# Kernel optimization log

Measured on AMD Instinct MI355X. Metric: run time of the kernel, lower is better.

Reference implementation:

```python
import jax, jax.numpy as jnp
import numpy as np

N_NODES = 50000
N_EDGES = 800000
IN_DIM, HIDDEN, Z_DIM = 32, 64, 32


def gcn_conv(x, W, b, src, dst, n):
    """PyG-style GCNConv: h = D^{-1/2}(A+I)D^{-1/2} (x W) + b."""
    h = x @ W  # [N, out]
    loop = jnp.arange(n, dtype=src.dtype)
    s = jnp.concatenate([src, loop])  # add self-loops
    d = jnp.concatenate([dst, loop])
    deg = jax.ops.segment_sum(jnp.ones(s.shape, h.dtype), d, num_segments=n)
    dinv = jax.lax.rsqrt(jnp.maximum(deg, jnp.asarray(1.0, h.dtype)))
    norm = dinv[s] * dinv[d]                       # [E+N]
    msg = h[s] * norm[:, None]                     # gather + scale
    out = jax.ops.segment_sum(msg, d, num_segments=n)  # scatter-add
    return out + b


def setup_inputs() -> dict:
    key = jax.random.key(0)
    ks = jax.random.split(key, 8)
    sc = lambda fan_in: 1.0 / np.sqrt(fan_in)
    x = jax.random.normal(ks[0], (N_NODES, IN_DIM), jnp.float32)
    edge_index = jax.random.randint(ks[1], (2, N_EDGES), 0, N_NODES, jnp.int64)
    W1 = jax.random.normal(ks[2], (IN_DIM, HIDDEN), jnp.float32) * sc(IN_DIM)
    b1 = jnp.zeros((HIDDEN,), jnp.float32)
    W2 = jax.random.normal(ks[3], (HIDDEN, HIDDEN), jnp.float32) * sc(HIDDEN)
    b2 = jnp.zeros((HIDDEN,), jnp.float32)
    W_mu = jax.random.normal(ks[4], (HIDDEN, Z_DIM), jnp.float32) * sc(HIDDEN)
    b_mu = jnp.zeros((Z_DIM,), jnp.float32)
    W_lv = jax.random.normal(ks[5], (HIDDEN, Z_DIM), jnp.float32) * sc(HIDDEN)
    b_lv = jnp.zeros((Z_DIM,), jnp.float32)
    eps = jax.random.normal(ks[6], (N_NODES, Z_DIM), jnp.float32)
    return {"x": x, "edge_index": edge_index, "W1": W1, "b1": b1, "W2": W2,
            "b2": b2, "W_mu": W_mu, "b_mu": b_mu, "W_lv": W_lv, "b_lv": b_lv,
            "eps": eps}


def reference(x, edge_index, W1, b1, W2, b2, W_mu, b_mu, W_lv, b_lv, eps):
    src, dst = edge_index[0], edge_index[1]
    n = x.shape[0]
    h = jax.nn.relu(gcn_conv(x, W1, b1, src, dst, n))
    h = jax.nn.relu(gcn_conv(h, W2, b2, src, dst, n))
    # dropout p=0.0 -> identity
    mu = gcn_conv(h, W_mu, b_mu, src, dst, n)
    logvar = gcn_conv(h, W_lv, b_lv, src, dst, n)
    z = mu + jnp.exp(0.5 * logvar) * eps  # reparametrize
    return (z, mu, logvar)
```

## Files before the change

kernel.cpp:

```cpp
#include <hip/hip_runtime.h>
#include <math.h>

#define N_NODES 50000
#define N_EDGES 800000
#define IN_DIM 32
#define HIDDEN 64
#define Z_DIM 32
#define SCAN_B 256
#define NB_SCAN ((N_NODES + SCAN_B - 1) / SCAN_B)
#define N_XCD 8
#define NPX ((N_NODES + N_XCD - 1) / N_XCD)
#define SLICE 2048
#define N_SLICE ((N_EDGES + SLICE - 1) / SLICE)
#define SCAT_B (N_SLICE * N_XCD)
#define FB 1024
#define CPAD 16

__device__ __forceinline__ unsigned short f2bf(float f) {
    unsigned int u = __float_as_uint(f);
    u += 0x7fffu + ((u >> 16) & 1u);
    return (unsigned short)(u >> 16);
}

__device__ __forceinline__ int detect64(const int* raw) {
    int lane = threadIdx.x & 63;
    int odd = raw[2 * lane + 1];
    unsigned long long b = __ballot(odd != 0);
    return (b == 0ULL) ? 1 : 0;
}

__device__ __forceinline__ void fma8(float w, uint4 f, float acc[8]) {
    acc[0] = fmaf(w, __uint_as_float(f.x << 16),         acc[0]);
    acc[1] = fmaf(w, __uint_as_float(f.x & 0xffff0000u), acc[1]);
    acc[2] = fmaf(w, __uint_as_float(f.y << 16),         acc[2]);
    acc[3] = fmaf(w, __uint_as_float(f.y & 0xffff0000u), acc[3]);
    acc[4] = fmaf(w, __uint_as_float(f.z << 16),         acc[4]);
    acc[5] = fmaf(w, __uint_as_float(f.z & 0xffff0000u), acc[5]);
    acc[6] = fmaf(w, __uint_as_float(f.w << 16),         acc[6]);
    acc[7] = fmaf(w, __uint_as_float(f.w & 0xffff0000u), acc[7]);
}
__device__ __forceinline__ void mul8(float w, uint4 f, float acc[8]) {
    acc[0] = w * __uint_as_float(f.x << 16);
    acc[1] = w * __uint_as_float(f.x & 0xffff0000u);
    acc[2] = w * __uint_as_float(f.y << 16);
    acc[3] = w * __uint_as_float(f.y & 0xffff0000u);
    acc[4] = w * __uint_as_float(f.z << 16);
    acc[5] = w * __uint_as_float(f.z & 0xffff0000u);
    acc[6] = w * __uint_as_float(f.w << 16);
    acc[7] = w * __uint_as_float(f.w & 0xffff0000u);
}

__global__ void prep_a_kernel(const float* __restrict__ x, unsigned short* __restrict__ xb,
                              const void* __restrict__ raw, ushort2* __restrict__ ep0,
                              int* __restrict__ cnt) {
    int is64 = detect64((const int*)raw);
    int i = blockIdx.x * 256 + threadIdx.x;
    if (i < N_NODES * IN_DIM) xb[i] = f2bf(x[i]);
    if (i < N_NODES * CPAD) cnt[i] = 0;
    if (i < N_EDGES) {
        int s, d;
        if (is64) {
            s = (int)((const long long*)raw)[i];
            d = (int)((const long long*)raw)[N_EDGES + i];
        } else {
            s = ((const int*)raw)[i];
            d = ((const int*)raw)[N_EDGES + i];
        }
        ep0[i] = make_ushort2((unsigned short)s, (unsigned short)d);
    }
}

__global__ __launch_bounds__(256) void hist_kernel(const ushort2* __restrict__ ep0,
                                                   int* __restrict__ cnt,
                                                   unsigned short* __restrict__ rank) {
    int xcd = blockIdx.x % N_XCD;
    int sl  = blockIdx.x / N_XCD;
    int lo  = xcd * NPX, hi = lo + NPX;
    int base = sl * SLICE;
#pragma unroll
    for (int j = 0; j < SLICE / 256; j++) {
        int e = base + j * 256 + threadIdx.x;
        if (e < N_EDGES) {
            int d = ep0[e].y;
            if (d >= lo && d < hi)
                rank[e] = (unsigned short)atomicAdd(&cnt[(size_t)d * CPAD], 1);
        }
    }
}

__global__ void scan1_kernel(const int* __restrict__ cnt, int* __restrict__ pre,
                             int* __restrict__ bsum, float* __restrict__ dinv) {
    __shared__ int s[SCAN_B];
    int t = threadIdx.x;
    int g = blockIdx.x * SCAN_B + t;
    int v = (g < N_NODES) ? cnt[(size_t)g * CPAD] : 0;
    if (g < N_NODES) dinv[g] = rsqrtf((float)(v + 1));
    s[t] = v;
    __syncthreads();
    for (int o = 1; o < SCAN_B; o <<= 1) {
        int add = (t >= o) ? s[t - o] : 0;
        __syncthreads();
        s[t] += add;
        __syncthreads();
    }
    if (g < N_NODES) pre[g] = s[t] - v;
    if (t == SCAN_B - 1) bsum[blockIdx.x] = s[t];
}

#define BSUM_SCAN_PROLOGUE(bsum, sb, sx)                                    \
    {                                                                       \
        int t_ = threadIdx.x;                                               \
        int bv_ = (t_ < NB_SCAN) ? bsum[t_] : 0;                            \
        sb[t_] = bv_;                                                       \
        __syncthreads();                                                    \
        for (int o_ = 1; o_ < 256; o_ <<= 1) {                              \
            int a_ = (t_ >= o_) ? sb[t_ - o_] : 0;                          \
            __syncthreads();                                                \
            sb[t_] += a_;                                                   \
            __syncthreads();                                                \
        }                                                                   \
        sx[t_] = sb[t_] - bv_;                                              \
        __syncthreads();                                                    \
    }

__global__ __launch_bounds__(256) void scatter_kernel(
        const ushort2* __restrict__ ep0, const unsigned short* __restrict__ rank,
        const int* __restrict__ pre, const int* __restrict__ bsum,
        const float* __restrict__ dinv, int2* __restrict__ ep) {
    __shared__ int sb[256];
    __shared__ int sx[256];
    BSUM_SCAN_PROLOGUE(bsum, sb, sx)
    int base = blockIdx.x * SLICE;
#pragma unroll
    for (int j = 0; j < SLICE / 256; j++) {
        int e = base + j * 256 + threadIdx.x;
        if (e < N_EDGES) {
            ushort2 sd = ep0[e];
            int d = sd.y;
            int p = pre[d] + sx[d >> 8] + (int)rank[e];
            int s = sd.x;
            ep[p] = make_int2(s, __float_as_int(dinv[s]));
        }
    }
}

__device__ __forceinline__ void agg64(int e0, int e1, int2 pr,
                                      const int2* __restrict__ ep,
                                      const uint4* __restrict__ g4,
                                      int2* eb, int lane, int gsel, int c,
                                      float acc[8]) {
    for (int b0 = e0; b0 < e1; b0 += 64) {
        int cnt = e1 - b0; cnt = cnt > 64 ? 64 : cnt;
        eb[lane] = pr;
        for (int j = 0; j < cnt; j += 16) {
            int2 ew0 = eb[j + gsel];
            int2 ew1 = eb[j + 8 + gsel];
            uint4 f0 = g4[(size_t)ew0.x * 8 + c];
            uint4 f1 = g4[(size_t)ew1.x * 8 + c];
            fma8(__int_as_float(ew0.y), f0, acc);
            fma8(__int_as_float(ew1.y), f1, acc);
        }
        if (b0 + 64 < e1) {
            pr = make_int2(0, 0);
            int idx = b0 + 64 + lane;
            if (idx < e1) pr = ep[idx];
        }
    }
}

__device__ __forceinline__ void agg32(int e0, int e1, int2 pr,
                                      const int2* __restrict__ ep,
                                      const uint4* __restrict__ x4,
                                      int2* eb, int lane, int gsel, int c,
                                      float acc[8]) {
    for (int b0 = e0; b0 < e1; b0 += 64) {
        int cnt = e1 - b0; cnt = cnt > 64 ? 64 : cnt;
        eb[lane] = pr;
        for (int j = 0; j < cnt; j += 32) {
            int2 ew0 = eb[j + gsel];
            int2 ew1 = eb[j + 16 + gsel];
            uint4 f0 = x4[(size_t)ew0.x * 4 + c];
            uint4 f1 = x4[(size_t)ew1.x * 4 + c];
            fma8(__int_as_float(ew0.y), f0, acc);
            fma8(__int_as_float(ew1.y), f1, acc);
        }
        if (b0 + 64 < e1) {
            pr = make_int2(0, 0);
            int idx = b0 + 64 + lane;
            if (idx < e1) pr = ep[idx];
        }
    }
}

__global__ __launch_bounds__(256) void fused_layer32_kernel(
        const int* __restrict__ pre, const int* __restrict__ bsum,
        const int2* __restrict__ ep, const float* __restrict__ dinv,
        const unsigned short* __restrict__ xb,
        const float* __restrict__ W1, const float* __restrict__ b1,
        unsigned short* __restrict__ out) {
    __shared__ int sb[256];
    __shared__ int sx[256];
    __shared__ int2 ebuf[4][64];
    __shared__ float sq[4][32];
    BSUM_SCAN_PROLOGUE(bsum, sb, sx)
    int lane = threadIdx.x & 63;
    int wav  = threadIdx.x >> 6;
    int gsel = lane >> 2;
    int c    = lane & 3;
    const uint4* x4 = (const uint4*)xb;
    int2* eb = &ebuf[wav][0];
    float wcol[IN_DIM];
#pragma unroll
    for (int k = 0; k < IN_DIM; k++) wcol[k] = W1[k * 64 + lane];
    float bb = b1[lane];
    int wid = __builtin_amdgcn_readfirstlane((int)((blockIdx.x * blockDim.x + threadIdx.x) >> 6));
    int nw  = (gridDim.x * blockDim.x) >> 6;
    int v = wid;
    if (v >= N_NODES) return;
    int e0 = pre[v] + sx[v >> 8];
    int e1 = (v + 1 < N_NODES) ? pre[v + 1] + sx[(v + 1) >> 8] : N_EDGES;
    float dv = dinv[v];
    uint4 hv = x4[(size_t)v * 4 + c];
    int2 pr = make_int2(0, 0);
    if (lane < e1 - e0) pr = ep[e0 + lane];
    while (v < N_NODES) {
        int vn = v + nw;
        int e0n = 0, e1n = 0;
        float dvn = 0.0f;
        uint4 hvn = make_uint4(0, 0, 0, 0);
        int2 prn = make_int2(0, 0);
        if (vn < N_NODES) {
            e0n = pre[vn] + sx[vn >> 8];
            e1n = (vn + 1 < N_NODES) ? pre[vn + 1] + sx[(vn + 1) >> 8] : N_EDGES;
            dvn = dinv[vn];
            hvn = x4[(size_t)vn * 4 + c];
            if (lane < e1n - e0n) prn = ep[e0n + lane];
        }
        float sv = (gsel == 0) ? dv : 0.0f;
        float acc[8];
        mul8(sv, hv, acc);
        agg32(e0, e1, pr, ep, x4, eb, lane, gsel, c, acc);
#pragma unroll
        for (int i = 0; i < 8; i++) {
            acc[i] += __shfl_xor(acc[i], 4);
            acc[i] += __shfl_xor(acc[i], 8);
            acc[i] += __shfl_xor(acc[i], 16);
            acc[i] += __shfl_xor(acc[i], 32);
        }
        if (lane < 4) {
            float4* qd = (float4*)(&sq[wav][lane * 8]);
            qd[0] = make_float4(dv * acc[0], dv * acc[1], dv * acc[2], dv * acc[3]);
            qd[1] = make_float4(dv * acc[4], dv * acc[5], dv * acc[6], dv * acc[7]);
        }
        float o0 = bb, o1 = 0.0f, o2 = 0.0f, o3 = 0.0f;
        const float4* q4 = (const float4*)(&sq[wav][0]);
#pragma unroll
        for (int k = 0; k < IN_DIM / 4; k++) {
            float4 tq = q4[k];
            o0 = fmaf(tq.x, wcol[4 * k + 0], o0);
            o1 = fmaf(tq.y, wcol[4 * k + 1], o1);
            o2 = fmaf(tq.z, wcol[4 * k + 2], o2);
            o3 = fmaf(tq.w, wcol[4 * k + 3], o3);
        }
        float o = (o0 + o1) + (o2 + o3);
        out[(size_t)v * 64 + lane] = f2bf(fmaxf(o, 0.0f));
        v = vn; e0 = e0n; e1 = e1n; dv = dvn; hv = hvn; pr = prn;
    }
}

__global__ __launch_bounds__(256) void fused_layer64_kernel(
        const int* __restrict__ pre, const int* __restrict__ bsum,
        const int2* __restrict__ ep, const float* __restrict__ dinv,
        const unsigned short* __restrict__ g,
        const float* __restrict__ W, const float* __restrict__ bias,
        unsigned short* __restrict__ out) {
    __shared__ int sb[256];
    __shared__ int sx[256];
    __shared__ int2 ebuf[4][64];
    __shared__ float sq[4][64];
    BSUM_SCAN_PROLOGUE(bsum, sb, sx)
    int lane = threadIdx.x & 63;
    int wav  = threadIdx.x >> 6;
    int gsel = lane >> 3;
    int c    = lane & 7;
    const uint4* g4 = (const uint4*)g;
    int2* eb = &ebuf[wav][0];
    float wcol[HIDDEN];
#pragma unroll
    for (int k = 0; k < HIDDEN; k++) wcol[k] = W[k * 64 + lane];
    float bb = bias[lane];
    int wid = __builtin_amdgcn_readfirstlane((int)((blockIdx.x * blockDim.x + threadIdx.x) >> 6));
    int nw  = (gridDim.x * blockDim.x) >> 6;
    int v = wid;
    if (v >= N_NODES) return;
    int e0 = pre[v] + sx[v >> 8];
    int e1 = (v + 1 < N_NODES) ? pre[v + 1] + sx[(v + 1) >> 8] : N_EDGES;
    float dv = dinv[v];
    uint4 hv = g4[(size_t)v * 8 + c];
    int2 pr = make_int2(0, 0);
    if (lane < e1 - e0) pr = ep[e0 + lane];
    while (v < N_NODES) {
        int vn = v + nw;
        int e0n = 0, e1n = 0;
        float dvn = 0.0f;
        uint4 hvn = make_uint4(0, 0, 0, 0);
        int2 prn = make_int2(0, 0);
        if (vn < N_NODES) {
            e0n = pre[vn] + sx[vn >> 8];
            e1n = (vn + 1 < N_NODES) ? pre[vn + 1] + sx[(vn + 1) >> 8] : N_EDGES;
            dvn = dinv[vn];
            hvn = g4[(size_t)vn * 8 + c];
            if (lane < e1n - e0n) prn = ep[e0n + lane];
        }
        float sv = (gsel == 0) ? dv : 0.0f;
        float acc[8];
        mul8(sv, hv, acc);
        agg64(e0, e1, pr, ep, g4, eb, lane, gsel, c, acc);
#pragma unroll
        for (int i = 0; i < 8; i++) {
            acc[i] += __shfl_xor(acc[i], 8);
            acc[i] += __shfl_xor(acc[i], 16);
            acc[i] += __shfl_xor(acc[i], 32);
        }
        if (lane < 8) {
            float4* qd = (float4*)(&sq[wav][lane * 8]);
            qd[0] = make_float4(dv * acc[0], dv * acc[1], dv * acc[2], dv * acc[3]);
            qd[1] = make_float4(dv * acc[4], dv * acc[5], dv * acc[6], dv * acc[7]);
        }
        float o0 = bb, o1 = 0.0f, o2 = 0.0f, o3 = 0.0f;
        const float4* q4 = (const float4*)(&sq[wav][0]);
#pragma unroll
        for (int k = 0; k < HIDDEN / 4; k++) {
            float4 tq = q4[k];
            o0 = fmaf(tq.x, wcol[4 * k + 0], o0);
            o1 = fmaf(tq.y, wcol[4 * k + 1], o1);
            o2 = fmaf(tq.z, wcol[4 * k + 2], o2);
            o3 = fmaf(tq.w, wcol[4 * k + 3], o3);
        }
        float o = (o0 + o1) + (o2 + o3);
        out[(size_t)v * 64 + lane] = f2bf(fmaxf(o, 0.0f));
        v = vn; e0 = e0n; e1 = e1n; dv = dvn; hv = hvn; pr = prn;
    }
}

__global__ __launch_bounds__(256) void fused_head_kernel(
        const int* __restrict__ pre, const int* __restrict__ bsum,
        const int2* __restrict__ ep, const float* __restrict__ dinv,
        const unsigned short* __restrict__ g,
        const float* __restrict__ Wmu, const float* __restrict__ Wlv,
        const float* __restrict__ bmu, const float* __restrict__ blv,
        const float* __restrict__ eps, float* __restrict__ outz) {
    __shared__ int sb[256];
    __shared__ int sx[256];
    __shared__ int2 ebuf[4][64];
    __shared__ float sq[4][64];
    BSUM_SCAN_PROLOGUE(bsum, sb, sx)
    int lane = threadIdx.x & 63;
    int wav  = threadIdx.x >> 6;
    int gsel = lane >> 3;
    int c    = lane & 7;
    int f = lane & 31;
    bool hi = lane >= 32;
    const uint4* g4 = (const uint4*)g;
    int2* eb = &ebuf[wav][0];
    float wcol[HIDDEN];
#pragma unroll
    for (int k = 0; k < HIDDEN; k++)
        wcol[k] = hi ? Wlv[k * 32 + f] : Wmu[k * 32 + f];
    float bb = hi ? blv[f] : bmu[f];
    float* z  = outz;
    float* mu = outz + (size_t)N_NODES * Z_DIM;
    float* lv = outz + 2 * (size_t)N_NODES * Z_DIM;
    int wid = __builtin_amdgcn_readfirstlane((int)((blockIdx.x * blockDim.x + threadIdx.x) >> 6));
    int nw  = (gridDim.x * blockDim.x) >> 6;
    int v = wid;
    if (v >= N_NODES) return;
    int e0 = pre[v] + sx[v >> 8];
    int e1 = (v + 1 < N_NODES) ? pre[v + 1] + sx[(v + 1) >> 8] : N_EDGES;
    float dv = dinv[v];
    uint4 hv = g4[(size_t)v * 8 + c];
    int2 pr = make_int2(0, 0);
    if (lane < e1 - e0) pr = ep[e0 + lane];
    while (v < N_NODES) {
        int vn = v + nw;
        int e0n = 0, e1n = 0;
        float dvn = 0.0f;
        uint4 hvn = make_uint4(0, 0, 0, 0);
        int2 prn = make_int2(0, 0);
        if (vn < N_NODES) {
            e0n = pre[vn] + sx[vn >> 8];
            e1n = (vn + 1 < N_NODES) ? pre[vn + 1] + sx[(vn + 1) >> 8] : N_EDGES;
            dvn = dinv[vn];
            hvn = g4[(size_t)vn * 8 + c];
            if (lane < e1n - e0n) prn = ep[e0n + lane];
        }
        float sv = (gsel == 0) ? dv : 0.0f;
        float acc[8];
        mul8(sv, hv, acc);
        agg64(e0, e1, pr, ep, g4, eb, lane, gsel, c, acc);
#pragma unroll
        for (int i = 0; i < 8; i++) {
            acc[i] += __shfl_xor(acc[i], 8);
            acc[i] += __shfl_xor(acc[i], 16);
            acc[i] += __shfl_xor(acc[i], 32);
        }
        if (lane < 8) {
            float4* qd = (float4*)(&sq[wav][lane * 8]);
            qd[0] = make_float4(dv * acc[0], dv * acc[1], dv * acc[2], dv * acc[3]);
            qd[1] = make_float4(dv * acc[4], dv * acc[5], dv * acc[6], dv * acc[7]);
        }
        float m0 = bb, m1 = 0.0f, m2 = 0.0f, m3 = 0.0f;
        const float4* q4 = (const float4*)(&sq[wav][0]);
#pragma unroll
        for (int k = 0; k < HIDDEN / 4; k++) {
            float4 tq = q4[k];
            m0 = fmaf(tq.x, wcol[4 * k + 0], m0);
            m1 = fmaf(tq.y, wcol[4 * k + 1], m1);
            m2 = fmaf(tq.z, wcol[4 * k + 2], m2);
            m3 = fmaf(tq.w, wcol[4 * k + 3], m3);
        }
        float m = (m0 + m1) + (m2 + m3);
        float ev = eps[(size_t)v * Z_DIM + f];
        float t  = expf(0.5f * m) * ev;
        float tlo = __shfl(t, lane | 32);
        size_t o = (size_t)v * Z_DIM + f;
        if (!hi) { mu[o] = m; z[o] = m + tlo; }
        else     { lv[o] = m; }
        v = vn; e0 = e0n; e1 = e1n; dv = dvn; hv = hvn; pr = prn;
    }
}

extern "C" void kernel_launch(void* const* d_in, const int* in_sizes, int n_in,
                              void* d_out, int out_size, void* d_ws, size_t ws_size,
                              hipStream_t stream) {
    const float* x   = (const float*)d_in[0];
    const void*  ei  = d_in[1];
    const float* W1  = (const float*)d_in[2];
    const float* b1  = (const float*)d_in[3];
    const float* W2  = (const float*)d_in[4];
    const float* b2  = (const float*)d_in[5];
    const float* Wmu = (const float*)d_in[6];
    const float* bmu = (const float*)d_in[7];
    const float* Wlv = (const float*)d_in[8];
    const float* blv = (const float*)d_in[9];
    const float* eps = (const float*)d_in[10];
    float* out = (float*)d_out;
    (void)in_sizes; (void)n_in; (void)out_size; (void)ws_size;

    char* ws = (char*)d_ws;
    size_t off = 0;
    auto alloc = [&](size_t bytes) -> void* {
        void* p = ws + off;
        off += (bytes + 255) & ~(size_t)255;
        return p;
    };
    int2*           ep     = (int2*)alloc(sizeof(int2) * N_EDGES);
    ushort2*        ep0    = (ushort2*)alloc(sizeof(ushort2) * N_EDGES);
    unsigned short* rank   = (unsigned short*)alloc(sizeof(short) * N_EDGES);
    int*            pre    = (int*)alloc(sizeof(int) * (N_NODES + 1));
    int*            cnt    = (int*)alloc(sizeof(int) * (size_t)N_NODES * CPAD);
    float*          dinv   = (float*)alloc(sizeof(float) * N_NODES);
    int*            bsum   = (int*)alloc(sizeof(int) * 256);
    unsigned short* xb     = (unsigned short*)alloc(sizeof(short) * (size_t)N_NODES * IN_DIM);
    unsigned short* G      = (unsigned short*)alloc(sizeof(short) * (size_t)N_NODES * HIDDEN);
    unsigned short* H      = (unsigned short*)alloc(sizeof(short) * (size_t)N_NODES * HIDDEN);

    prep_a_kernel<<<(N_NODES * IN_DIM + 255) / 256, 256, 0, stream>>>(x, xb, ei, ep0, cnt);
    hist_kernel<<<SCAT_B, 256, 0, stream>>>(ep0, cnt, rank);
    scan1_kernel<<<NB_SCAN, SCAN_B, 0, stream>>>(cnt, pre, bsum, dinv);
    scatter_kernel<<<N_SLICE, 256, 0, stream>>>(ep0, rank, pre, bsum, dinv, ep);
    fused_layer32_kernel<<<FB, 256, 0, stream>>>(pre, bsum, ep, dinv, xb, W1, b1, H);
    fused_layer64_kernel<<<FB, 256, 0, stream>>>(pre, bsum, ep, dinv, H, W2, b2, G);
    fused_head_kernel<<<FB, 256, 0, stream>>>(pre, bsum, ep, dinv, G, Wmu, Wlv, bmu, blv, eps, out);
}
```

Measured before the change: 249.1 us.

## Map multiple nodes per wavefront and finalize row pointers in a separate scan kernel

Each layer kernel used to process one node per wavefront in a grid-stride loop, staging edges through LDS. Now a sub-group of lanes (4 or 8) handles one node, so each wave covers 8 or 16 nodes, with edge indices broadcast by shuffles. The dense transform is batched over those nodes with weights held in LDS instead of registers. A new scan23 kernel finalizes global row pointers once, so the per-block bsum prefix-scan prologue in every consumer kernel is removed. This targets low lane utilization on low-degree nodes and the repeated scans, at the cost of load imbalance from the per-wave max degree and one extra launch.

```diff
diff --git a/kernel.cpp b/kernel.cpp
--- a/kernel.cpp
+++ b/kernel.cpp
@@ -13,8 +13,14 @@
 #define SLICE 2048
 #define N_SLICE ((N_EDGES + SLICE - 1) / SLICE)
 #define SCAT_B (N_SLICE * N_XCD)
-#define FB 1024
 #define CPAD 16
+
+#define NPW64 8
+#define NPB64 (4 * NPW64)
+#define FB64 ((N_NODES + NPB64 - 1) / NPB64)
+#define NPW32 16
+#define NPB32 (4 * NPW32)
+#define FB32 ((N_NODES + NPB32 - 1) / NPB32)
 
 __device__ __forceinline__ unsigned short f2bf(float f) {
     unsigned int u = __float_as_uint(f);
@@ -88,7 +94,7 @@
     }
 }
 
-__global__ void scan1_kernel(const int* __restrict__ cnt, int* __restrict__ pre,
+__global__ void scan1_kernel(const int* __restrict__ cnt, int* __restrict__ rowptr,
                              int* __restrict__ bsum, float* __restrict__ dinv) {
     __shared__ int s[SCAN_B];
     int t = threadIdx.x;
@@ -103,330 +109,309 @@
         s[t] += add;
         __syncthreads();
     }
-    if (g < N_NODES) pre[g] = s[t] - v;
+    if (g < N_NODES) rowptr[g] = s[t] - v;
     if (t == SCAN_B - 1) bsum[blockIdx.x] = s[t];
 }
 
-#define BSUM_SCAN_PROLOGUE(bsum, sb, sx)                                    \
-    {                                                                       \
-        int t_ = threadIdx.x;                                               \
-        int bv_ = (t_ < NB_SCAN) ? bsum[t_] : 0;                            \
-        sb[t_] = bv_;                                                       \
-        __syncthreads();                                                    \
-        for (int o_ = 1; o_ < 256; o_ <<= 1) {                              \
-            int a_ = (t_ >= o_) ? sb[t_ - o_] : 0;                          \
-            __syncthreads();                                                \
-            sb[t_] += a_;                                                   \
-            __syncthreads();                                                \
-        }                                                                   \
-        sx[t_] = sb[t_] - bv_;                                              \
-        __syncthreads();                                                    \
-    }
+__global__ void scan23_kernel(int* __restrict__ rowptr, const int* __restrict__ bsum) {
+    __shared__ int s[256];
+    int t = threadIdx.x;
+    int v = (t < NB_SCAN) ? bsum[t] : 0;
+    s[t] = v;
+    __syncthreads();
+    for (int o = 1; o < 256; o <<= 1) {
+        int add = (t >= o) ? s[t - o] : 0;
+        __syncthreads();
+        s[t] += add;
+        __syncthreads();
+    }
+    int excl = s[blockIdx.x] - bsum[blockIdx.x];
+    int g = blockIdx.x * SCAN_B + t;
+    if (g < N_NODES) rowptr[g] += excl;
+    if (g == 0) rowptr[N_NODES] = N_EDGES;
+}
 
 __global__ __launch_bounds__(256) void scatter_kernel(
         const ushort2* __restrict__ ep0, const unsigned short* __restrict__ rank,
-        const int* __restrict__ pre, const int* __restrict__ bsum,
-        const float* __restrict__ dinv, int2* __restrict__ ep) {
-    __shared__ int sb[256];
-    __shared__ int sx[256];
-    BSUM_SCAN_PROLOGUE(bsum, sb, sx)
+        const int* __restrict__ rowptr, const float* __restrict__ dinv,
+        int2* __restrict__ ep) {
     int base = blockIdx.x * SLICE;
 #pragma unroll
     for (int j = 0; j < SLICE / 256; j++) {
         int e = base + j * 256 + threadIdx.x;
         if (e < N_EDGES) {
             ushort2 sd = ep0[e];
-            int d = sd.y;
-            int p = pre[d] + sx[d >> 8] + (int)rank[e];
+            int p = rowptr[sd.y] + (int)rank[e];
             int s = sd.x;
             ep[p] = make_int2(s, __float_as_int(dinv[s]));
         }
     }
 }
 
-__device__ __forceinline__ void agg64(int e0, int e1, int2 pr,
-                                      const int2* __restrict__ ep,
-                                      const uint4* __restrict__ g4,
-                                      int2* eb, int lane, int gsel, int c,
-                                      float acc[8]) {
-    for (int b0 = e0; b0 < e1; b0 += 64) {
-        int cnt = e1 - b0; cnt = cnt > 64 ? 64 : cnt;
-        eb[lane] = pr;
-        for (int j = 0; j < cnt; j += 16) {
-            int2 ew0 = eb[j + gsel];
-            int2 ew1 = eb[j + 8 + gsel];
-            uint4 f0 = g4[(size_t)ew0.x * 8 + c];
-            uint4 f1 = g4[(size_t)ew1.x * 8 + c];
-            fma8(__int_as_float(ew0.y), f0, acc);
-            fma8(__int_as_float(ew1.y), f1, acc);
-        }
-        if (b0 + 64 < e1) {
-            pr = make_int2(0, 0);
-            int idx = b0 + 64 + lane;
-            if (idx < e1) pr = ep[idx];
-        }
-    }
-}
-
-__device__ __forceinline__ void agg32(int e0, int e1, int2 pr,
-                                      const int2* __restrict__ ep,
-                                      const uint4* __restrict__ x4,
-                                      int2* eb, int lane, int gsel, int c,
-                                      float acc[8]) {
-    for (int b0 = e0; b0 < e1; b0 += 64) {
-        int cnt = e1 - b0; cnt = cnt > 64 ? 64 : cnt;
-        eb[lane] = pr;
-        for (int j = 0; j < cnt; j += 32) {
-            int2 ew0 = eb[j + gsel];
-            int2 ew1 = eb[j + 16 + gsel];
-            uint4 f0 = x4[(size_t)ew0.x * 4 + c];
-            uint4 f1 = x4[(size_t)ew1.x * 4 + c];
-            fma8(__int_as_float(ew0.y), f0, acc);
-            fma8(__int_as_float(ew1.y), f1, acc);
-        }
-        if (b0 + 64 < e1) {
-            pr = make_int2(0, 0);
-            int idx = b0 + 64 + lane;
-            if (idx < e1) pr = ep[idx];
-        }
-    }
-}
-
 __global__ __launch_bounds__(256) void fused_layer32_kernel(
-        const int* __restrict__ pre, const int* __restrict__ bsum,
-        const int2* __restrict__ ep, const float* __restrict__ dinv,
-        const unsigned short* __restrict__ xb,
+        const int* __restrict__ rowptr, const int2* __restrict__ ep,
+        const float* __restrict__ dinv, const unsigned short* __restrict__ xb,
         const float* __restrict__ W1, const float* __restrict__ b1,
         unsigned short* __restrict__ out) {
-    __shared__ int sb[256];
-    __shared__ int sx[256];
-    __shared__ int2 ebuf[4][64];
-    __shared__ float sq[4][32];
-    BSUM_SCAN_PROLOGUE(bsum, sb, sx)
+    __shared__ __align__(16) float wlds[IN_DIM * 64];
+    __shared__ __align__(16) float sq[4][NPW32][IN_DIM];
+    for (int i = threadIdx.x; i < IN_DIM * 64; i += 256) wlds[i] = W1[i];
+    __syncthreads();
     int lane = threadIdx.x & 63;
     int wav  = threadIdx.x >> 6;
-    int gsel = lane >> 2;
-    int c    = lane & 3;
+    int grp  = lane >> 2;
+    int li   = lane & 3;
+    int gb   = lane & 60;
     const uint4* x4 = (const uint4*)xb;
-    int2* eb = &ebuf[wav][0];
-    float wcol[IN_DIM];
-#pragma unroll
-    for (int k = 0; k < IN_DIM; k++) wcol[k] = W1[k * 64 + lane];
     float bb = b1[lane];
-    int wid = __builtin_amdgcn_readfirstlane((int)((blockIdx.x * blockDim.x + threadIdx.x) >> 6));
-    int nw  = (gridDim.x * blockDim.x) >> 6;
-    int v = wid;
-    if (v >= N_NODES) return;
-    int e0 = pre[v] + sx[v >> 8];
-    int e1 = (v + 1 < N_NODES) ? pre[v + 1] + sx[(v + 1) >> 8] : N_EDGES;
-    float dv = dinv[v];
-    uint4 hv = x4[(size_t)v * 4 + c];
+    int vbase = ((int)blockIdx.x * 4 + wav) * NPW32;
+    int v = vbase + grp;
+    bool ok = v < N_NODES;
+    int e0 = 0, e1 = 0;
+    float dv = 0.0f;
+    uint4 hv = make_uint4(0, 0, 0, 0);
+    if (ok) {
+        e0 = rowptr[v]; e1 = rowptr[v + 1];
+        dv = dinv[v];
+        hv = x4[(size_t)v * 4 + li];
+    }
+    int deg = e1 - e0;
+    float acc[8];
+    mul8(dv, hv, acc);
+    int mx = deg;
+    mx = max(mx, __shfl_xor(mx, 4));
+    mx = max(mx, __shfl_xor(mx, 8));
+    mx = max(mx, __shfl_xor(mx, 16));
+    mx = max(mx, __shfl_xor(mx, 32));
+    mx = __builtin_amdgcn_readfirstlane(mx);
     int2 pr = make_int2(0, 0);
-    if (lane < e1 - e0) pr = ep[e0 + lane];
-    while (v < N_NODES) {
-        int vn = v + nw;
-        int e0n = 0, e1n = 0;
-        float dvn = 0.0f;
-        uint4 hvn = make_uint4(0, 0, 0, 0);
+    if (li < deg) pr = ep[e0 + li];
+    for (int j0 = 0; j0 < mx; j0 += 4) {
         int2 prn = make_int2(0, 0);
-        if (vn < N_NODES) {
-            e0n = pre[vn] + sx[vn >> 8];
-            e1n = (vn + 1 < N_NODES) ? pre[vn + 1] + sx[(vn + 1) >> 8] : N_EDGES;
-            dvn = dinv[vn];
-            hvn = x4[(size_t)vn * 4 + c];
-            if (lane < e1n - e0n) prn = ep[e0n + lane];
-        }
-        float sv = (gsel == 0) ? dv : 0.0f;
-        float acc[8];
-        mul8(sv, hv, acc);
-        agg32(e0, e1, pr, ep, x4, eb, lane, gsel, c, acc);
-#pragma unroll
-        for (int i = 0; i < 8; i++) {
-            acc[i] += __shfl_xor(acc[i], 4);
-            acc[i] += __shfl_xor(acc[i], 8);
-            acc[i] += __shfl_xor(acc[i], 16);
-            acc[i] += __shfl_xor(acc[i], 32);
-        }
-        if (lane < 4) {
-            float4* qd = (float4*)(&sq[wav][lane * 8]);
-            qd[0] = make_float4(dv * acc[0], dv * acc[1], dv * acc[2], dv * acc[3]);
-            qd[1] = make_float4(dv * acc[4], dv * acc[5], dv * acc[6], dv * acc[7]);
-        }
-        float o0 = bb, o1 = 0.0f, o2 = 0.0f, o3 = 0.0f;
-        const float4* q4 = (const float4*)(&sq[wav][0]);
-#pragma unroll
-        for (int k = 0; k < IN_DIM / 4; k++) {
-            float4 tq = q4[k];
-            o0 = fmaf(tq.x, wcol[4 * k + 0], o0);
-            o1 = fmaf(tq.y, wcol[4 * k + 1], o1);
-            o2 = fmaf(tq.z, wcol[4 * k + 2], o2);
-            o3 = fmaf(tq.w, wcol[4 * k + 3], o3);
-        }
-        float o = (o0 + o1) + (o2 + o3);
-        out[(size_t)v * 64 + lane] = f2bf(fmaxf(o, 0.0f));
-        v = vn; e0 = e0n; e1 = e1n; dv = dvn; hv = hvn; pr = prn;
+        int idxn = j0 + 4 + li;
+        if (idxn < deg) prn = ep[e0 + idxn];
+#pragma unroll
+        for (int jj = 0; jj < 4; jj++) {
+            int ss = __shfl(pr.x, gb + jj);
+            int ww = __shfl(pr.y, gb + jj);
+            bool act = (j0 + jj) < deg;
+            ss = act ? ss : 0;
+            float w = act ? __int_as_float(ww) : 0.0f;
+            uint4 f = x4[(size_t)ss * 4 + li];
+            fma8(w, f, acc);
+        }
+        pr = prn;
+    }
+    {
+        float4* qd = (float4*)&sq[wav][grp][li * 8];
+        qd[0] = make_float4(dv * acc[0], dv * acc[1], dv * acc[2], dv * acc[3]);
+        qd[1] = make_float4(dv * acc[4], dv * acc[5], dv * acc[6], dv * acc[7]);
+    }
+    float o[NPW32];
+#pragma unroll
+    for (int n = 0; n < NPW32; n++) o[n] = bb;
+#pragma unroll
+    for (int k4 = 0; k4 < IN_DIM / 4; k4++) {
+        float w0 = wlds[(k4 * 4 + 0) * 64 + lane];
+        float w1 = wlds[(k4 * 4 + 1) * 64 + lane];
+        float w2 = wlds[(k4 * 4 + 2) * 64 + lane];
+        float w3 = wlds[(k4 * 4 + 3) * 64 + lane];
+#pragma unroll
+        for (int n = 0; n < NPW32; n++) {
+            float4 q = *(const float4*)&sq[wav][n][k4 * 4];
+            o[n] = fmaf(q.x, w0, o[n]);
+            o[n] = fmaf(q.y, w1, o[n]);
+            o[n] = fmaf(q.z, w2, o[n]);
+            o[n] = fmaf(q.w, w3, o[n]);
+        }
+    }
+#pragma unroll
+    for (int n = 0; n < NPW32; n++) {
+        int vv = vbase + n;
+        if (vv < N_NODES) out[(size_t)vv * 64 + lane] = f2bf(fmaxf(o[n], 0.0f));
     }
 }
 
 __global__ __launch_bounds__(256) void fused_layer64_kernel(
-        const int* __restrict__ pre, const int* __restrict__ bsum,
-        const int2* __restrict__ ep, const float* __restrict__ dinv,
-        const unsigned short* __restrict__ g,
+        const int* __restrict__ rowptr, const int2* __restrict__ ep,
+        const float* __restrict__ dinv, const unsigned short* __restrict__ g,
         const float* __restrict__ W, const float* __restrict__ bias,
         unsigned short* __restrict__ out) {
-    __shared__ int sb[256];
-    __shared__ int sx[256];
-    __shared__ int2 ebuf[4][64];
-    __shared__ float sq[4][64];
-    BSUM_SCAN_PROLOGUE(bsum, sb, sx)
+    __shared__ __align__(16) float wlds[HIDDEN * 64];
+    __shared__ __align__(16) float sq[4][NPW64][HIDDEN];
+    for (int i = threadIdx.x; i < HIDDEN * 64; i += 256) wlds[i] = W[i];
+    __syncthreads();
     int lane = threadIdx.x & 63;
     int wav  = threadIdx.x >> 6;
-    int gsel = lane >> 3;
-    int c    = lane & 7;
+    int grp  = lane >> 3;
+    int li   = lane & 7;
+    int gb   = lane & 56;
     const uint4* g4 = (const uint4*)g;
-    int2* eb = &ebuf[wav][0];
-    float wcol[HIDDEN];
-#pragma unroll
-    for (int k = 0; k < HIDDEN; k++) wcol[k] = W[k * 64 + lane];
     float bb = bias[lane];
-    int wid = __builtin_amdgcn_readfirstlane((int)((blockIdx.x * blockDim.x + threadIdx.x) >> 6));
-    int nw  = (gridDim.x * blockDim.x) >> 6;
-    int v = wid;
-    if (v >= N_NODES) return;
-    int e0 = pre[v] + sx[v >> 8];
-    int e1 = (v + 1 < N_NODES) ? pre[v + 1] + sx[(v + 1) >> 8] : N_EDGES;
-    float dv = dinv[v];
-    uint4 hv = g4[(size_t)v * 8 + c];
+    int vbase = ((int)blockIdx.x * 4 + wav) * NPW64;
+    int v = vbase + grp;
+    bool ok = v < N_NODES;
+    int e0 = 0, e1 = 0;
+    float dv = 0.0f;
+    uint4 hv = make_uint4(0, 0, 0, 0);
+    if (ok) {
+        e0 = rowptr[v]; e1 = rowptr[v + 1];
+        dv = dinv[v];
+        hv = g4[(size_t)v * 8 + li];
+    }
+    int deg = e1 - e0;
+    float acc[8];
+    mul8(dv, hv, acc);
+    int mx = deg;
+    mx = max(mx, __shfl_xor(mx, 8));
+    mx = max(mx, __shfl_xor(mx, 16));
+    mx = max(mx, __shfl_xor(mx, 32));
+    mx = __builtin_amdgcn_readfirstlane(mx);
     int2 pr = make_int2(0, 0);
-    if (lane < e1 - e0) pr = ep[e0 + lane];
-    while (v < N_NODES) {
-        int vn = v + nw;
-        int e0n = 0, e1n = 0;
-        float dvn = 0.0f;
-        uint4 hvn = make_uint4(0, 0, 0, 0);
+    if (li < deg) pr = ep[e0 + li];
+    for (int j0 = 0; j0 < mx; j0 += 8) {
         int2 prn = make_int2(0, 0);
-        if (vn < N_NODES) {
-            e0n = pre[vn] + sx[vn >> 8];
-            e1n = (vn + 1 < N_NODES) ? pre[vn + 1] + sx[(vn + 1) >> 8] : N_EDGES;
-            dvn = dinv[vn];
-            hvn = g4[(size_t)vn * 8 + c];
-            if (lane < e1n - e0n) prn = ep[e0n + lane];
-        }
-        float sv = (gsel == 0) ? dv : 0.0f;
-        float acc[8];
-        mul8(sv, hv, acc);
-        agg64(e0, e1, pr, ep, g4, eb, lane, gsel, c, acc);
-#pragma unroll
-        for (int i = 0; i < 8; i++) {
-            acc[i] += __shfl_xor(acc[i], 8);
-            acc[i] += __shfl_xor(acc[i], 16);
-            acc[i] += __shfl_xor(acc[i], 32);
-        }
-        if (lane < 8) {
-            float4* qd = (float4*)(&sq[wav][lane * 8]);
-            qd[0] = make_float4(dv * acc[0], dv * acc[1], dv * acc[2], dv * acc[3]);
-            qd[1] = make_float4(dv * acc[4], dv * acc[5], dv * acc[6], dv * acc[7]);
-        }
-        float o0 = bb, o1 = 0.0f, o2 = 0.0f, o3 = 0.0f;
-        const float4* q4 = (const float4*)(&sq[wav][0]);
-#pragma unroll
-        for (int k = 0; k < HIDDEN / 4; k++) {
-            float4 tq = q4[k];
-            o0 = fmaf(tq.x, wcol[4 * k + 0], o0);
-            o1 = fmaf(tq.y, wcol[4 * k + 1], o1);
-            o2 = fmaf(tq.z, wcol[4 * k + 2], o2);
-            o3 = fmaf(tq.w, wcol[4 * k + 3], o3);
-        }
-        float o = (o0 + o1) + (o2 + o3);
-        out[(size_t)v * 64 + lane] = f2bf(fmaxf(o, 0.0f));
-        v = vn; e0 = e0n; e1 = e1n; dv = dvn; hv = hvn; pr = prn;
+        int idxn = j0 + 8 + li;
+        if (idxn < deg) prn = ep[e0 + idxn];
+#pragma unroll
+        for (int jj = 0; jj < 8; jj++) {
+            int ss = __shfl(pr.x, gb + jj);
+            int ww = __shfl(pr.y, gb + jj);
+            bool act = (j0 + jj) < deg;
+            ss = act ? ss : 0;
+            float w = act ? __int_as_float(ww) : 0.0f;
+            uint4 f = g4[(size_t)ss * 8 + li];
+            fma8(w, f, acc);
+        }
+        pr = prn;
+    }
+    {
+        float4* qd = (float4*)&sq[wav][grp][li * 8];
+        qd[0] = make_float4(dv * acc[0], dv * acc[1], dv * acc[2], dv * acc[3]);
+        qd[1] = make_float4(dv * acc[4], dv * acc[5], dv * acc[6], dv * acc[7]);
+    }
+    float o[NPW64];
+#pragma unroll
+    for (int n = 0; n < NPW64; n++) o[n] = bb;
+#pragma unroll
+    for (int k4 = 0; k4 < HIDDEN / 4; k4++) {
+        float w0 = wlds[(k4 * 4 + 0) * 64 + lane];
+        float w1 = wlds[(k4 * 4 + 1) * 64 + lane];
+        float w2 = wlds[(k4 * 4 + 2) * 64 + lane];
+        float w3 = wlds[(k4 * 4 + 3) * 64 + lane];
+#pragma unroll
+        for (int n = 0; n < NPW64; n++) {
+            float4 q = *(const float4*)&sq[wav][n][k4 * 4];
+            o[n] = fmaf(q.x, w0, o[n]);
+            o[n] = fmaf(q.y, w1, o[n]);
+            o[n] = fmaf(q.z, w2, o[n]);
+            o[n] = fmaf(q.w, w3, o[n]);
+        }
+    }
+#pragma unroll
+    for (int n = 0; n < NPW64; n++) {
+        int vv = vbase + n;
+        if (vv < N_NODES) out[(size_t)vv * 64 + lane] = f2bf(fmaxf(o[n], 0.0f));
     }
 }
 
 __global__ __launch_bounds__(256) void fused_head_kernel(
-        const int* __restrict__ pre, const int* __restrict__ bsum,
-        const int2* __restrict__ ep, const float* __restrict__ dinv,
-        const unsigned short* __restrict__ g,
+        const int* __restrict__ rowptr, const int2* __restrict__ ep,
+        const float* __restrict__ dinv, const unsigned short* __restrict__ g,
         const float* __restrict__ Wmu, const float* __restrict__ Wlv,
         const float* __restrict__ bmu, const float* __restrict__ blv,
         const float* __restrict__ eps, float* __restrict__ outz) {
-    __shared__ int sb[256];
-    __shared__ int sx[256];
-    __shared__ int2 ebuf[4][64];
-    __shared__ float sq[4][64];
-    BSUM_SCAN_PROLOGUE(bsum, sb, sx)
+    __shared__ __align__(16) float wlds[HIDDEN * 64];
+    __shared__ __align__(16) float sq[4][NPW64][HIDDEN];
+    for (int i = threadIdx.x; i < HIDDEN * 64; i += 256) {
+        int k = i >> 6, col = i & 63;
+        wlds[i] = (col < 32) ? Wmu[k * 32 + col] : Wlv[k * 32 + (col - 32)];
+    }
+    __syncthreads();
     int lane = threadIdx.x & 63;
     int wav  = threadIdx.x >> 6;
-    int gsel = lane >> 3;
-    int c    = lane & 7;
-    int f = lane & 31;
-    bool hi = lane >= 32;
+    int grp  = lane >> 3;
+    int li   = lane & 7;
+    int gb   = lane & 56;
+    int f    = lane & 31;
+    bool hi  = lane >= 32;
     const uint4* g4 = (const uint4*)g;
-    int2* eb = &ebuf[wav][0];
-    float wcol[HIDDEN];
-#pragma unroll
-    for (int k = 0; k < HIDDEN; k++)
-        wcol[k] = hi ? Wlv[k * 32 + f] : Wmu[k * 32 + f];
     float bb = hi ? blv[f] : bmu[f];
     float* z  = outz;
     float* mu = outz + (size_t)N_NODES * Z_DIM;
     float* lv = outz + 2 * (size_t)N_NODES * Z_DIM;
-    int wid = __builtin_amdgcn_readfirstlane((int)((blockIdx.x * blockDim.x + threadIdx.x) >> 6));
-    int nw  = (gridDim.x * blockDim.x) >> 6;
-    int v = wid;
-    if (v >= N_NODES) return;
-    int e0 = pre[v] + sx[v >> 8];
-    int e1 = (v + 1 < N_NODES) ? pre[v + 1] + sx[(v + 1) >> 8] : N_EDGES;
-    float dv = dinv[v];
-    uint4 hv = g4[(size_t)v * 8 + c];
+    int vbase = ((int)blockIdx.x * 4 + wav) * NPW64;
+    int v = vbase + grp;
+    bool ok = v < N_NODES;
+    int e0 = 0, e1 = 0;
+    float dv = 0.0f;
+    uint4 hv = make_uint4(0, 0, 0, 0);
+    if (ok) {
+        e0 = rowptr[v]; e1 = rowptr[v + 1];
+        dv = dinv[v];
+        hv = g4[(size_t)v * 8 + li];
+    }
+    int deg = e1 - e0;
+    float acc[8];
+    mul8(dv, hv, acc);
+    int mx = deg;
+    mx = max(mx, __shfl_xor(mx, 8));
+    mx = max(mx, __shfl_xor(mx, 16));
+    mx = max(mx, __shfl_xor(mx, 32));
+    mx = __builtin_amdgcn_readfirstlane(mx);
     int2 pr = make_int2(0, 0);
-    if (lane < e1 - e0) pr = ep[e0 + lane];
-    while (v < N_NODES) {
-        int vn = v + nw;
-        int e0n = 0, e1n = 0;
-        float dvn = 0.0f;
-        uint4 hvn = make_uint4(0, 0, 0, 0);
+    if (li < deg) pr = ep[e0 + li];
+    for (int j0 = 0; j0 < mx; j0 += 8) {
         int2 prn = make_int2(0, 0);
-        if (vn < N_NODES) {
-            e0n = pre[vn] + sx[vn >> 8];
-            e1n = (vn + 1 < N_NODES) ? pre[vn + 1] + sx[(vn + 1) >> 8] : N_EDGES;
-            dvn = dinv[vn];
-            hvn = g4[(size_t)vn * 8 + c];
-            if (lane < e1n - e0n) prn = ep[e0n + lane];
-        }
-        float sv = (gsel == 0) ? dv : 0.0f;
-        float acc[8];
-        mul8(sv, hv, acc);
-        agg64(e0, e1, pr, ep, g4, eb, lane, gsel, c, acc);
-#pragma unroll
-        for (int i = 0; i < 8; i++) {
-            acc[i] += __shfl_xor(acc[i], 8);
-            acc[i] += __shfl_xor(acc[i], 16);
-            acc[i] += __shfl_xor(acc[i], 32);
-        }
-        if (lane < 8) {
-            float4* qd = (float4*)(&sq[wav][lane * 8]);
-            qd[0] = make_float4(dv * acc[0], dv * acc[1], dv * acc[2], dv * acc[3]);
-            qd[1] = make_float4(dv * acc[4], dv * acc[5], dv * acc[6], dv * acc[7]);
-        }
-        float m0 = bb, m1 = 0.0f, m2 = 0.0f, m3 = 0.0f;
-        const float4* q4 = (const float4*)(&sq[wav][0]);
-#pragma unroll
-        for (int k = 0; k < HIDDEN / 4; k++) {
-            float4 tq = q4[k];
-            m0 = fmaf(tq.x, wcol[4 * k + 0], m0);
-            m1 = fmaf(tq.y, wcol[4 * k + 1], m1);
-            m2 = fmaf(tq.z, wcol[4 * k + 2], m2);
-            m3 = fmaf(tq.w, wcol[4 * k + 3], m3);
-        }
-        float m = (m0 + m1) + (m2 + m3);
-        float ev = eps[(size_t)v * Z_DIM + f];
-        float t  = expf(0.5f * m) * ev;
-        float tlo = __shfl(t, lane | 32);
-        size_t o = (size_t)v * Z_DIM + f;
-        if (!hi) { mu[o] = m; z[o] = m + tlo; }
-        else     { lv[o] = m; }
-        v = vn; e0 = e0n; e1 = e1n; dv = dvn; hv = hvn; pr = prn;
+        int idxn = j0 + 8 + li;
+        if (idxn < deg) prn = ep[e0 + idxn];
+#pragma unroll
+        for (int jj = 0; jj < 8; jj++) {
+            int ss = __shfl(pr.x, gb + jj);
+            int ww = __shfl(pr.y, gb + jj);
+            bool act = (j0 + jj) < deg;
+            ss = act ? ss : 0;
+            float w = act ? __int_as_float(ww) : 0.0f;
+            uint4 fr = g4[(size_t)ss * 8 + li];
+            fma8(w, fr, acc);
+        }
+        pr = prn;
+    }
+    {
+        float4* qd = (float4*)&sq[wav][grp][li * 8];
+        qd[0] = make_float4(dv * acc[0], dv * acc[1], dv * acc[2], dv * acc[3]);
+        qd[1] = make_float4(dv * acc[4], dv * acc[5], dv * acc[6], dv * acc[7]);
+    }
+    float o[NPW64];
+#pragma unroll
+    for (int n = 0; n < NPW64; n++) o[n] = bb;
+#pragma unroll
+    for (int k4 = 0; k4 < HIDDEN / 4; k4++) {
+        float w0 = wlds[(k4 * 4 + 0) * 64 + lane];
+        float w1 = wlds[(k4 * 4 + 1) * 64 + lane];
+        float w2 = wlds[(k4 * 4 + 2) * 64 + lane];
+        float w3 = wlds[(k4 * 4 + 3) * 64 + lane];
+#pragma unroll
+        for (int n = 0; n < NPW64; n++) {
+            float4 q = *(const float4*)&sq[wav][n][k4 * 4];
+            o[n] = fmaf(q.x, w0, o[n]);
+            o[n] = fmaf(q.y, w1, o[n]);
+            o[n] = fmaf(q.z, w2, o[n]);
+            o[n] = fmaf(q.w, w3, o[n]);
+        }
+    }
+#pragma unroll
+    for (int n = 0; n < NPW64; n++) {
+        int vv = vbase + n;
+        if (vv < N_NODES) {
+            float m  = o[n];
+            float ev = eps[(size_t)vv * Z_DIM + f];
+            float t  = expf(0.5f * m) * ev;
+            float tlo = __shfl(t, lane | 32);
+            size_t oo = (size_t)vv * Z_DIM + f;
+            if (!hi) { mu[oo] = m; z[oo] = m + tlo; }
+            else     { lv[oo] = m; }
+        }
     }
 }
 
@@ -457,7 +442,7 @@
     int2*           ep     = (int2*)alloc(sizeof(int2) * N_EDGES);
     ushort2*        ep0    = (ushort2*)alloc(sizeof(ushort2) * N_EDGES);
     unsigned short* rank   = (unsigned short*)alloc(sizeof(short) * N_EDGES);
-    int*            pre    = (int*)alloc(sizeof(int) * (N_NODES + 1));
+    int*            rowptr = (int*)alloc(sizeof(int) * (N_NODES + 1));
     int*            cnt    = (int*)alloc(sizeof(int) * (size_t)N_NODES * CPAD);
     float*          dinv   = (float*)alloc(sizeof(float) * N_NODES);
     int*            bsum   = (int*)alloc(sizeof(int) * 256);
@@ -467,9 +452,10 @@
 
     prep_a_kernel<<<(N_NODES * IN_DIM + 255) / 256, 256, 0, stream>>>(x, xb, ei, ep0, cnt);
     hist_kernel<<<SCAT_B, 256, 0, stream>>>(ep0, cnt, rank);
-    scan1_kernel<<<NB_SCAN, SCAN_B, 0, stream>>>(cnt, pre, bsum, dinv);
-    scatter_kernel<<<N_SLICE, 256, 0, stream>>>(ep0, rank, pre, bsum, dinv, ep);
-    fused_layer32_kernel<<<FB, 256, 0, stream>>>(pre, bsum, ep, dinv, xb, W1, b1, H);
-    fused_layer64_kernel<<<FB, 256, 0, stream>>>(pre, bsum, ep, dinv, H, W2, b2, G);
-    fused_head_kernel<<<FB, 256, 0, stream>>>(pre, bsum, ep, dinv, G, Wmu, Wlv, bmu, blv, eps, out);
-}
+    scan1_kernel<<<NB_SCAN, SCAN_B, 0, stream>>>(cnt, rowptr, bsum, dinv);
+    scan23_kernel<<<NB_SCAN, SCAN_B, 0, stream>>>(rowptr, bsum);
+    scatter_kernel<<<N_SLICE, 256, 0, stream>>>(ep0, rank, rowptr, dinv, ep);
+    fused_layer32_kernel<<<FB32, 256, 0, stream>>>(rowptr, ep, dinv, xb, W1, b1, H);
+    fused_layer64_kernel<<<FB64, 256, 0, stream>>>(rowptr, ep, dinv, H, W2, b2, G);
+    fused_head_kernel<<<FB64, 256, 0, stream>>>(rowptr, ep, dinv, G, Wmu, Wlv, bmu, blv, eps, out);
+}
```

New measurement: 360.4 us. +44.7%, slower.
